# Optimization experiments

Hardware: AMD Instinct MI355X
Metric: run time of the kernel (lower is better)

## Reference

```python
import jax, jax.numpy as jnp
import numpy as np

B, G, NB, NC = 1024, 28, 2, 20
THR_CONF = 3.0
THR_NMS = 0.3
K = 4096            # fixed top-k detection slots (jit-friendly padding)
NEG = jnp.float32(-1e30)


def setup_inputs() -> dict:
    key = jax.random.key(0)
    k1, k2, k3 = jax.random.split(key, 3)
    return {
        "p_boxes": jax.random.normal(k1, (B, G, G, NB * 4), dtype=jnp.float32),
        "p_confs": jax.random.normal(k2, (B, G, G, NB), dtype=jnp.float32),
        "p_clses": jax.random.normal(k3, (B, G, G, NC), dtype=jnp.float32),
    }


def _decode_topk(p_boxes, p_confs, p_clses):
    # boxes: (B,G,G,NB,4) with (offx, offy, w, h) per box slot
    boxes = p_boxes.reshape(B, G, G, NB, 4)
    col = jnp.arange(G, dtype=jnp.float32)
    row = jnp.arange(G, dtype=jnp.float32)
    # offxy2xy: xy = (offxy + colrow) / num_grid  (dim1=row, dim2=col per torch.where order)
    cx = (boxes[..., 0] + col[None, None, :, None]) / G
    cy = (boxes[..., 1] + row[None, :, None, None]) / G
    w, h = boxes[..., 2], boxes[..., 3]
    # xywh2ltrb
    ltrb = jnp.stack([cx - w * 0.5, cy - h * 0.5, cx + w * 0.5, cy + h * 0.5], axis=-1)
    # label = argmax over classes + 1, shared by both box slots of a cell
    labels = jnp.argmax(p_clses, axis=-1) + 1                       # (B,G,G)
    labels = jnp.broadcast_to(labels[..., None], (B, G, G, NB))
    bids = jnp.broadcast_to(jnp.arange(B)[:, None, None, None], (B, G, G, NB))
    valid = p_confs > THR_CONF

    N = B * G * G * NB
    scores_masked = jnp.where(valid, p_confs, NEG).reshape(N)
    topv, topi = jax.lax.top_k(scores_masked, K)                    # sorted desc
    boxes_k = ltrb.reshape(N, 4)[topi]
    labels_k = labels.reshape(N)[topi]
    bids_k = bids.reshape(N)[topi]
    scores_k = p_confs.reshape(N)[topi]
    valid_k = topv > THR_CONF
    return bids_k, boxes_k, labels_k, scores_k, valid_k


def _iou_matrix(b):
    # b: (K,4) ltrb -> (K,K) pairwise IoU
    lt = jnp.maximum(b[:, None, :2], b[None, :, :2])
    rb = jnp.minimum(b[:, None, 2:], b[None, :, 2:])
    wh = jnp.clip(rb - lt, 0.0)
    inter = wh[..., 0] * wh[..., 1]
    area = jnp.clip(b[:, 2] - b[:, 0], 0.0) * jnp.clip(b[:, 3] - b[:, 1], 0.0)
    union = area[:, None] + area[None, :] - inter
    return inter / jnp.maximum(union, 1e-9)


def _nms(boxes, groups, valid):
    # per-(batch,label) NMS via group equality mask; boxes pre-sorted by score desc
    same = groups[:, None] == groups[None, :]
    suppress = same & (_iou_matrix(boxes) > THR_NMS)                # (K,K)
    idx = jnp.arange(K)

    def body(i, keep):
        sup = jnp.any(keep & suppress[:, i] & (idx < i))
        return keep.at[i].set(valid[i] & ~sup)

    return jax.lax.fori_loop(0, K, body, jnp.zeros((K,), dtype=bool))


def reference(p_boxes, p_confs, p_clses):
    bids, boxes, labels, scores, valid = _decode_topk(p_boxes, p_confs, p_clses)
    groups = bids * (NC + 1) + labels
    keep = _nms(boxes, groups, valid)
    # padded outputs of fixed size K; `keep` marks surviving detections
    return bids, boxes, labels, scores, keep
```

## Files before the change

kernel.cpp:

```cpp
#include <hip/hip_runtime.h>
#include <stdint.h>

#define B_    1024
#define G_    28
#define NB_   2
#define NC_   20
#define KK    4096
#define NTOT  (B_*G_*G_*NB_)
#define THRC  3.0f
#define THRN  0.3f
#define SORT_N 8192
#define NGRP  (B_*(NC_+1))
#define GCAP  8
#define RB    256
#define NRB2  (SORT_N/RB)
#define CPT   16

#define WS_CNT   0
#define WS_GCNT  256
#define WS_ZERO_BYTES (256 + NGRP*4)
#define WS_KEYS  86272
#define WS_GMEM  (WS_KEYS + SORT_N*8)

typedef unsigned long long u64;

__global__ void k_zero(int4* __restrict__ p) {
    int t = blockIdx.x * blockDim.x + threadIdx.x;
    if (t < WS_ZERO_BYTES / 16) p[t] = make_int4(0, 0, 0, 0);
}

__global__ void k_collect(const float4* __restrict__ conf4, const float* __restrict__ clses,
                          u64* __restrict__ keys, int* cnt,
                          int* __restrict__ gcnt, u64* __restrict__ gmem) {
    int t = blockIdx.x * blockDim.x + threadIdx.x;
    int lane = threadIdx.x & 63;
    float cc[CPT];
    #pragma unroll
    for (int q = 0; q < CPT / 4; ++q) {
        float4 v = conf4[t * (CPT / 4) + q];
        cc[q * 4 + 0] = v.x; cc[q * 4 + 1] = v.y;
        cc[q * 4 + 2] = v.z; cc[q * 4 + 3] = v.w;
    }
    int nh = 0;
    #pragma unroll
    for (int u = 0; u < CPT; ++u) nh += (cc[u] > THRC);
    u64 act = __ballot(nh > 0);
    if (act) {
        int incl = nh;
        #pragma unroll
        for (int off = 1; off < 64; off <<= 1) {
            int v = __shfl_up(incl, off);
            if (lane >= off) incl += v;
        }
        int tot = __shfl(incl, 63);
        int base = 0;
        if (lane == 0) base = atomicAdd(cnt, tot);
        base = __shfl(base, 0);
        int pos = base + incl - nh;
        int fb = t * CPT;
        #pragma unroll
        for (int u = 0; u < CPT; ++u) {
            if (cc[u] > THRC) {
                int idx = fb + u;
                unsigned b = __float_as_uint(cc[u]);
                b = (b & 0x80000000u) ? ~b : (b | 0x80000000u);
                u64 key = ((u64)b << 32) | (u64)(0xFFFFFFFFu - (unsigned)idx);
                if (pos < SORT_N) keys[pos] = key;
                pos++;
                int cell = idx >> 1;
                const float4* cp4 = (const float4*)(clses + (size_t)cell * NC_);
                float best = -3.4e38f; int lab = 0;
                #pragma unroll
                for (int q = 0; q < 5; ++q) {
                    float4 cv = cp4[q];
                    float vv[4] = {cv.x, cv.y, cv.z, cv.w};
                    #pragma unroll
                    for (int w = 0; w < 4; ++w) {
                        int ci = q * 4 + w;
                        if (vv[w] > best) { best = vv[w]; lab = ci; }
                    }
                }
                int g = (cell / (G_ * G_)) * (NC_ + 1) + (lab + 1);
                int p2 = atomicAdd(&gcnt[g], 1);
                if (p2 < GCAP) gmem[(size_t)g * GCAP + p2] = key;
            }
        }
    }
}

__device__ inline float4 box_of(int idx, const float* __restrict__ boxes) {
    int nb = idx & 1;
    int cell = idx >> 1;
    int gx = cell % G_;
    int gy = (cell / G_) % G_;
    float4 bv = *(const float4*)(boxes + (size_t)cell * (NB_ * 4) + nb * 4);
    float cx = (bv.x + (float)gx) / (float)G_;
    float cy = (bv.y + (float)gy) / (float)G_;
    return make_float4(cx - bv.z * 0.5f, cy - bv.w * 0.5f,
                       cx + bv.z * 0.5f, cy + bv.w * 0.5f);
}

struct Dec { int b; int lab; };
__device__ inline Dec decode_write(int slot, int idx, float score,
                                   const float* __restrict__ boxes,
                                   const float* __restrict__ clses,
                                   float* __restrict__ out) {
    int cell = idx >> 1;
    int b = cell / (G_ * G_);
    float4 lt = box_of(idx, boxes);
    const float4* cp4 = (const float4*)(clses + (size_t)cell * NC_);
    float best = -3.4e38f; int lab = 0;
    #pragma unroll
    for (int q = 0; q < 5; ++q) {
        float4 cv = cp4[q];
        float vv[4] = {cv.x, cv.y, cv.z, cv.w};
        #pragma unroll
        for (int u = 0; u < 4; ++u) {
            int ci = q * 4 + u;
            if (vv[u] > best) { best = vv[u]; lab = ci; }
        }
    }
    lab += 1;
    out[slot] = (float)b;
    *(float4*)(out + KK + 4*slot) = lt;
    out[5*KK + slot] = (float)lab;
    out[6*KK + slot] = score;
    out[7*KK + slot] = 0.0f;
    Dec d; d.b = b; d.lab = lab;
    return d;
}

__global__ void __launch_bounds__(RB) k_rankdec(const float* __restrict__ boxes,
                                                const float4* __restrict__ conf4,
                                                const float* __restrict__ conf,
                                                const float* __restrict__ clses,
                                                const int* __restrict__ cnt,
                                                const u64* __restrict__ keys,
                                                float* __restrict__ out,
                                                const int* __restrict__ gcnt,
                                                const u64* __restrict__ gmem) {
    int tid = threadIdx.x;
    int lane = tid & 63;
    int Vtot = min(cnt[0], SORT_N);
    int V = min(Vtot, KK);

    if (blockIdx.x == NRB2) {
        __shared__ int wsum[4];
        int M = KK - V;
        if (M <= 0) return;
        unsigned mask = 0;
        int base = tid * 32;
        #pragma unroll
        for (int q = 0; q < 8; ++q) {
            float4 cv = conf4[tid * 8 + q];
            mask |= (unsigned)(!(cv.x > THRC)) << (q * 4 + 0);
            mask |= (unsigned)(!(cv.y > THRC)) << (q * 4 + 1);
            mask |= (unsigned)(!(cv.z > THRC)) << (q * 4 + 2);
            mask |= (unsigned)(!(cv.w > THRC)) << (q * 4 + 3);
        }
        int c = __popc(mask);
        int incl = c;
        #pragma unroll
        for (int off = 1; off < 64; off <<= 1) {
            int v = __shfl_up(incl, off);
            if (lane >= off) incl += v;
        }
        int wid = tid >> 6;
        if (lane == 63) wsum[wid] = incl;
        __syncthreads();
        int wbase = 0;
        for (int w = 0; w < wid; ++w) wbase += wsum[w];
        int p = wbase + incl - c;
        unsigned m = mask;
        while (m) {
            int u = __builtin_ctz(m);
            if (p < M) {
                int idx = base + u;
                decode_write(V + p, idx, conf[idx], boxes, clses, out);
            }
            p++;
            m &= m - 1;
        }
        return;
    }

    __shared__ u64 sk[SORT_N];
    if (blockIdx.x * RB >= Vtot) return;
    const ulonglong2* keys2 = (const ulonglong2*)keys;
    for (int i = tid; i * 2 < Vtot; i += RB) {
        ulonglong2 kv = keys2[i];
        sk[2 * i]     = kv.x;
        sk[2 * i + 1] = kv.y;
    }
    __syncthreads();
    int t = blockIdx.x * RB + tid;
    if (t >= Vtot) return;
    u64 k0 = sk[t];
    int r = 0, j = 0;
    int lim = Vtot & ~7;
    for (; j < lim; j += 8) {
        r += (int)(sk[j+0] > k0) + (int)(sk[j+1] > k0)
           + (int)(sk[j+2] > k0) + (int)(sk[j+3] > k0)
           + (int)(sk[j+4] > k0) + (int)(sk[j+5] > k0)
           + (int)(sk[j+6] > k0) + (int)(sk[j+7] > k0);
    }
    for (; j < Vtot; ++j) r += (int)(sk[j] > k0);
    if (r >= KK) return;
    int idx = (int)(0xFFFFFFFFu - (unsigned)(k0 & 0xFFFFFFFFull));
    float score = __uint_as_float((unsigned)(k0 >> 32) ^ 0x80000000u);
    Dec d = decode_write(r, idx, score, boxes, clses, out);

    int g = d.b * (NC_ + 1) + d.lab;
    int m = min(gcnt[g], GCAP);
    u64 mem[GCAP];
    for (int i = 0; i < m; ++i) mem[i] = gmem[(size_t)g * GCAP + i];
    for (int i = 1; i < m; ++i) {
        u64 v = mem[i]; int q = i - 1;
        while (q >= 0 && mem[q] < v) { mem[q + 1] = mem[q]; --q; }
        mem[q + 1] = v;
    }
    bool survive;
    if (m <= 1) {
        survive = true;
    } else {
        int own = 0;
        float4 bx[GCAP]; float ar[GCAP];
        for (int i = 0; i < m; ++i) {
            if (mem[i] == k0) own = i;
            int mi = (int)(0xFFFFFFFFu - (unsigned)(mem[i] & 0xFFFFFFFFull));
            bx[i] = box_of(mi, boxes);
            ar[i] = fmaxf(bx[i].z - bx[i].x, 0.f) * fmaxf(bx[i].w - bx[i].y, 0.f);
        }
        unsigned keepm = 0;
        for (int i = 0; i < m; ++i) {
            bool sup = false;
            for (int q = 0; q < i; ++q) {
                if ((keepm >> q) & 1u) {
                    float lx = fmaxf(bx[i].x, bx[q].x), ly = fmaxf(bx[i].y, bx[q].y);
                    float rx = fminf(bx[i].z, bx[q].z), ry = fminf(bx[i].w, bx[q].w);
                    float inter = fmaxf(rx - lx, 0.f) * fmaxf(ry - ly, 0.f);
                    float uni = ar[i] + ar[q] - inter;
                    if (inter / fmaxf(uni, 1e-9f) > THRN) sup = true;
                }
            }
            if (!sup) keepm |= 1u << i;
        }
        survive = (keepm >> own) & 1u;
    }
    if (survive) out[7*KK + r] = 1.0f;
}

extern "C" void kernel_launch(void* const* d_in, const int* in_sizes, int n_in,
                              void* d_out, int out_size, void* d_ws, size_t ws_size,
                              hipStream_t stream) {
    const float* p_boxes = (const float*)d_in[0];
    const float* p_confs = (const float*)d_in[1];
    const float* p_clses = (const float*)d_in[2];
    float* out = (float*)d_out;
    char* ws = (char*)d_ws;

    int*  cnt   = (int*) (ws + WS_CNT);
    int*  gcnt  = (int*) (ws + WS_GCNT);
    u64*  keys  = (u64*) (ws + WS_KEYS);
    u64*  gmem  = (u64*) (ws + WS_GMEM);

    k_zero   <<<(WS_ZERO_BYTES / 16 + 255) / 256, 256, 0, stream>>>((int4*)ws);
    k_collect<<<NTOT / CPT / 256, 256, 0, stream>>>((const float4*)p_confs, p_clses,
                                                    keys, cnt, gcnt, gmem);
    k_rankdec<<<NRB2 + 1, RB, 0, stream>>>(p_boxes, (const float4*)p_confs, p_confs,
                                           p_clses, cnt, keys, out, gcnt, gmem);
}
```

Measured before the change: 58.27 us.

## Split rank counting across four wavefronts per key with shared-memory reduction

The rank-by-counting kernel now gives each block 64 keys instead of 256. The four wavefronts each count over a quarter of the comparison range, and the partial counts are summed through shared memory. This lets more blocks run the O(V^2) rank pass in parallel and shortens each thread's serial loop. In exchange, every block still loads the full key array into shared memory, so there is four times as much redundant shared-memory fill, plus an extra barrier per block. Only one wavefront per block continues into the decode and NMS phase.

```diff
diff --git a/kernel.cpp b/kernel.cpp
--- a/kernel.cpp
+++ b/kernel.cpp
@@ -13,7 +13,8 @@
 #define NGRP  (B_*(NC_+1))
 #define GCAP  8
 #define RB    256
-#define NRB2  (SORT_N/RB)
+#define KPB   64
+#define NRBF  (SORT_N/KPB)
 #define CPT   16
 
 #define WS_CNT   0
@@ -144,7 +145,7 @@
     int Vtot = min(cnt[0], SORT_N);
     int V = min(Vtot, KK);
 
-    if (blockIdx.x == NRB2) {
+    if (blockIdx.x == NRBF) {
         __shared__ int wsum[4];
         int M = KK - V;
         if (M <= 0) return;
@@ -185,7 +186,8 @@
     }
 
     __shared__ u64 sk[SORT_N];
-    if (blockIdx.x * RB >= Vtot) return;
+    __shared__ int partial[KPB][5];
+    if (blockIdx.x * KPB >= Vtot) return;
     const ulonglong2* keys2 = (const ulonglong2*)keys;
     for (int i = tid; i * 2 < Vtot; i += RB) {
         ulonglong2 kv = keys2[i];
@@ -193,19 +195,33 @@
         sk[2 * i + 1] = kv.y;
     }
     __syncthreads();
-    int t = blockIdx.x * RB + tid;
-    if (t >= Vtot) return;
+
+    int k = tid & (KPB - 1);
+    int q = tid >> 6;
+    int t = blockIdx.x * KPB + k;
+    int chunk = (Vtot + 3) >> 2;
+    int j0 = q * chunk;
+    int j1 = min(j0 + chunk, Vtot);
+    int r4 = 0;
+    if (t < Vtot) {
+        u64 k0 = sk[t];
+        int j = j0;
+        int lim = j0 + ((j1 - j0) & ~7);
+        for (; j < lim; j += 8) {
+            r4 += (int)(sk[j+0] > k0) + (int)(sk[j+1] > k0)
+                + (int)(sk[j+2] > k0) + (int)(sk[j+3] > k0)
+                + (int)(sk[j+4] > k0) + (int)(sk[j+5] > k0)
+                + (int)(sk[j+6] > k0) + (int)(sk[j+7] > k0);
+        }
+        for (; j < j1; ++j) r4 += (int)(sk[j] > k0);
+    }
+    partial[k][q] = r4;
+    __syncthreads();
+
+    if (tid >= KPB || t >= Vtot) return;
+    int r = partial[tid][0] + partial[tid][1] + partial[tid][2] + partial[tid][3];
+    if (r >= KK) return;
     u64 k0 = sk[t];
-    int r = 0, j = 0;
-    int lim = Vtot & ~7;
-    for (; j < lim; j += 8) {
-        r += (int)(sk[j+0] > k0) + (int)(sk[j+1] > k0)
-           + (int)(sk[j+2] > k0) + (int)(sk[j+3] > k0)
-           + (int)(sk[j+4] > k0) + (int)(sk[j+5] > k0)
-           + (int)(sk[j+6] > k0) + (int)(sk[j+7] > k0);
-    }
-    for (; j < Vtot; ++j) r += (int)(sk[j] > k0);
-    if (r >= KK) return;
     int idx = (int)(0xFFFFFFFFu - (unsigned)(k0 & 0xFFFFFFFFull));
     float score = __uint_as_float((unsigned)(k0 >> 32) ^ 0x80000000u);
     Dec d = decode_write(r, idx, score, boxes, clses, out);
@@ -215,9 +231,9 @@
     u64 mem[GCAP];
     for (int i = 0; i < m; ++i) mem[i] = gmem[(size_t)g * GCAP + i];
     for (int i = 1; i < m; ++i) {
-        u64 v = mem[i]; int q = i - 1;
-        while (q >= 0 && mem[q] < v) { mem[q + 1] = mem[q]; --q; }
-        mem[q + 1] = v;
+        u64 v = mem[i]; int qq = i - 1;
+        while (qq >= 0 && mem[qq] < v) { mem[qq + 1] = mem[qq]; --qq; }
+        mem[qq + 1] = v;
     }
     bool survive;
     if (m <= 1) {
@@ -234,12 +250,12 @@
         unsigned keepm = 0;
         for (int i = 0; i < m; ++i) {
             bool sup = false;
-            for (int q = 0; q < i; ++q) {
-                if ((keepm >> q) & 1u) {
-                    float lx = fmaxf(bx[i].x, bx[q].x), ly = fmaxf(bx[i].y, bx[q].y);
-                    float rx = fminf(bx[i].z, bx[q].z), ry = fminf(bx[i].w, bx[q].w);
+            for (int qq = 0; qq < i; ++qq) {
+                if ((keepm >> qq) & 1u) {
+                    float lx = fmaxf(bx[i].x, bx[qq].x), ly = fmaxf(bx[i].y, bx[qq].y);
+                    float rx = fminf(bx[i].z, bx[qq].z), ry = fminf(bx[i].w, bx[qq].w);
                     float inter = fmaxf(rx - lx, 0.f) * fmaxf(ry - ly, 0.f);
-                    float uni = ar[i] + ar[q] - inter;
+                    float uni = ar[i] + ar[qq] - inter;
                     if (inter / fmaxf(uni, 1e-9f) > THRN) sup = true;
                 }
             }
@@ -267,6 +283,6 @@
     k_zero   <<<(WS_ZERO_BYTES / 16 + 255) / 256, 256, 0, stream>>>((int4*)ws);
     k_collect<<<NTOT / CPT / 256, 256, 0, stream>>>((const float4*)p_confs, p_clses,
                                                     keys, cnt, gcnt, gmem);
-    k_rankdec<<<NRB2 + 1, RB, 0, stream>>>(p_boxes, (const float4*)p_confs, p_confs,
+    k_rankdec<<<NRBF + 1, RB, 0, stream>>>(p_boxes, (const float4*)p_confs, p_confs,
                                            p_clses, cnt, keys, out, gcnt, gmem);
 }
```

Result: faster. 48.14 us (-17.4%).
